# Kernel optimization log

Measured on AMD Instinct MI355X. Metric: run time of the kernel, lower is better.

## Reference

```python
import jax, jax.numpy as jnp
import numpy as np

N_ATOMS = 16384
N_SPECIES = 4
D_IN = 2880      # len(species)^2 * max_radial^2 * (max_angular+1) = 16*36*5
H = 256
N_STRUCTURES = 64


def setup_inputs() -> dict:
    key = jax.random.key(0)
    ks = jax.random.split(key, 9)
    features = jax.random.normal(ks[0], (N_ATOMS, D_IN), dtype=jnp.float32)
    # per-species MLP (MLPMap): 2 hidden layers with SiLU, then LinearMap -> 1
    w1 = jax.random.normal(ks[1], (N_SPECIES, D_IN, H), dtype=jnp.float32) * 0.02
    b1 = jax.random.normal(ks[2], (N_SPECIES, H), dtype=jnp.float32) * 0.02
    w2 = jax.random.normal(ks[3], (N_SPECIES, H, H), dtype=jnp.float32) * 0.05
    b2 = jax.random.normal(ks[4], (N_SPECIES, H), dtype=jnp.float32) * 0.02
    w_last = jax.random.normal(ks[5], (N_SPECIES, H), dtype=jnp.float32) * 0.05
    b_last = jax.random.normal(ks[6], (N_SPECIES,), dtype=jnp.float32) * 0.02
    comp_weights = jax.random.normal(ks[7], (N_SPECIES,), dtype=jnp.float32)
    # atoms are species-contiguous (TensorMap blocks); structures sorted
    structure_idx = jnp.sort(
        jax.random.randint(ks[8], (N_ATOMS,), 0, N_STRUCTURES, dtype=jnp.int32)
    )
    return {
        "features": features,
        "w1": w1, "b1": b1, "w2": w2, "b2": b2,
        "w_last": w_last, "b_last": b_last,
        "comp_weights": comp_weights,
        "structure_idx": structure_idx,
    }


def reference(features, w1, b1, w2, b2, w_last, b_last, comp_weights, structure_idx):
    S = N_SPECIES
    n_per = N_ATOMS // S
    # species-partitioned blocks: [S, n_per, D] — grouped GEMM form of the
    # per-species ModuleDict loop in MLPMap / LinearMap
    xs = features.reshape(S, n_per, D_IN)
    h = jax.nn.silu(jnp.einsum("snd,sdh->snh", xs, w1) + b1[:, None, :])
    h = jax.nn.silu(jnp.einsum("snh,shk->snk", h, w2) + b2[:, None, :])
    # LinearMap: per-species Linear(H, 1)
    e = jnp.einsum("snh,sh->sn", h, w_last) + b_last[:, None]  # [S, n_per]
    # apply_composition_contribution: add per-species composition weight
    species_per_atom = jnp.repeat(jnp.arange(S), n_per)
    atomic_energy = e.reshape(N_ATOMS) + comp_weights[species_per_atom]
    # keys_to_samples + sum_over_samples(['center','species_center'])
    total = jax.ops.segment_sum(atomic_energy, structure_idx,
                                num_segments=N_STRUCTURES)
    return total[:, None]  # [n_structures, 1] energy block
```

## Files before the change

### kernel.cpp

```cpp
#include <hip/hip_runtime.h>
#include <hip/hip_bf16.h>

#define D_IN    2880
#define HDIM    256
#define NSPEC   4
#define NATOMS  16384
#define NSTRUCT 64
#define NT1     45
#define NT2     4
#define BM      64

typedef __attribute__((ext_vector_type(4))) float f32x4;
typedef __attribute__((ext_vector_type(8))) short s16x8;
typedef __attribute__((ext_vector_type(4))) unsigned short u16x4;

__device__ __forceinline__ short f2bf(float f) {
    return (short)__builtin_bit_cast(unsigned short, __float2bfloat16(f));
}

template<int RDIM>
__global__ void pack_w(const float* __restrict__ w, unsigned short* __restrict__ wp) {
    __shared__ unsigned short T[64][264];
    const int kt = blockIdx.x, s = blockIdx.y;
    const int t = threadIdx.x;
    const float* src = w + ((size_t)s * RDIM + kt * 64) * HDIM;
#pragma unroll
    for (int i = 0; i < 16; ++i) {
        const int row = i * 4 + (t >> 6);
        const int c4 = (t & 63) * 4;
        f32x4 v = *(const f32x4*)(src + (size_t)row * HDIM + c4);
        u16x4 u;
        u[0] = (unsigned short)f2bf(v[0]); u[1] = (unsigned short)f2bf(v[1]);
        u[2] = (unsigned short)f2bf(v[2]); u[3] = (unsigned short)f2bf(v[3]);
        *(u16x4*)&T[row][c4] = u;
    }
    __syncthreads();
    unsigned short* dst = wp + ((size_t)s * (RDIM / 64) + kt) * 16384;
    const int l = t & 63;
#pragma unroll
    for (int it = 0; it < 8; ++it) {
        const int c = (t >> 6) + it * 4;
        const int hq = c >> 1, kk = c & 1;
        s16x8 vv;
#pragma unroll
        for (int e = 0; e < 8; ++e)
            vv[e] = (short)T[kk * 32 + (l >> 4) * 8 + e][hq * 16 + (l & 15)];
        *(s16x8*)(dst + (size_t)c * 512 + l * 8) = vv;
    }
}

__device__ __forceinline__ int aswz(int row, int colbyte) {
    return row * 128 + (colbyte ^ ((row & 7) << 4));
}
__device__ __forceinline__ int hswz(int row, int colbyte) {
    return row * 512 + (colbyte ^ ((row & 7) << 4));
}

__global__ __launch_bounds__(512, 2)
void fused_mlp(const float* __restrict__ feat,
               const unsigned short* __restrict__ w1p,
               const float* __restrict__ b1,
               const unsigned short* __restrict__ w2p,
               const float* __restrict__ b2,
               const float* __restrict__ w_last,
               const float* __restrict__ b_last,
               const float* __restrict__ comp_w,
               const int* __restrict__ sidx,
               float* __restrict__ out)
{
    __shared__ __align__(16) char Ab[2][8192];
    __shared__ __align__(16) char Hb[BM * 512];
    __shared__ float ered[4][BM];

    const int tid  = threadIdx.x;
    const int lane = tid & 63;
    const int wv   = tid >> 6;
    const int wr   = wv >> 2, wc = wv & 3;
    const int lrow = lane & 15, lq = lane >> 4;
    const int g    = blockIdx.x;
    const int s    = (g & 7) >> 1;
    const int mloc = ((g >> 3) << 1) | (g & 1);
    const int row0 = s * (NATOMS / NSPEC) + mloc * BM;

    const float* Ag = feat + (size_t)row0 * D_IN;
    const unsigned short* B1 = w1p + (size_t)s * NT1 * 16384;
    const unsigned short* B2 = w2p + (size_t)s * NT2 * 16384;

    const int ar  = tid >> 3;
    const int acb = (tid & 7) * 16;
    const int awo = aswz(ar, acb);

    f32x4 acc[2][4];
#pragma unroll
    for (int i = 0; i < 2; ++i)
#pragma unroll
        for (int j = 0; j < 4; ++j) acc[i][j] = (f32x4){0.f, 0.f, 0.f, 0.f};

    {
        const float* ap = Ag + (size_t)ar * D_IN + (tid & 7) * 8;
        f32x4 v0 = *(const f32x4*)ap;
        f32x4 v1 = *(const f32x4*)(ap + 4);
        s16x8 pw;
        pw[0]=f2bf(v0[0]); pw[1]=f2bf(v0[1]); pw[2]=f2bf(v0[2]); pw[3]=f2bf(v0[3]);
        pw[4]=f2bf(v1[0]); pw[5]=f2bf(v1[1]); pw[6]=f2bf(v1[2]); pw[7]=f2bf(v1[3]);
        *(s16x8*)(&Ab[0][0] + awo) = pw;
    }
    s16x8 Bf[2][4][2];
#pragma unroll
    for (int j = 0; j < 4; ++j)
#pragma unroll
        for (int kk = 0; kk < 2; ++kk)
            Bf[0][j][kk] = *(const s16x8*)(B1 + ((wc * 4 + j) * 2 + kk) * 512 + lane * 8);
    __syncthreads();

#pragma unroll 2
    for (int kt = 0; kt < NT1; ++kt) {
        const int cb = kt & 1, nb = cb ^ 1;
        const bool hn = (kt + 1) < NT1;
        f32x4 a0, a1;
        if (hn) {
            const float* ap = Ag + (size_t)ar * D_IN + (kt + 1) * 64 + (tid & 7) * 8;
            a0 = *(const f32x4*)ap;
            a1 = *(const f32x4*)(ap + 4);
#pragma unroll
            for (int j = 0; j < 4; ++j)
#pragma unroll
                for (int kk = 0; kk < 2; ++kk)
                    Bf[nb][j][kk] = *(const s16x8*)(B1 + ((size_t)(kt + 1) * 32 + (wc * 4 + j) * 2 + kk) * 512 + lane * 8);
        }
        s16x8 af[2][2];
#pragma unroll
        for (int i = 0; i < 2; ++i)
#pragma unroll
            for (int kk = 0; kk < 2; ++kk)
                af[i][kk] = *(const s16x8*)(&Ab[cb][0] + aswz(wr * 32 + i * 16 + lrow, kk * 64 + lq * 16));
#pragma unroll
        for (int kk = 0; kk < 2; ++kk)
#pragma unroll
            for (int i = 0; i < 2; ++i)
#pragma unroll
                for (int j = 0; j < 4; ++j)
                    acc[i][j] = __builtin_amdgcn_mfma_f32_16x16x32_bf16(af[i][kk], Bf[cb][j][kk], acc[i][j], 0, 0, 0);
        if (hn) {
            s16x8 pw;
            pw[0]=f2bf(a0[0]); pw[1]=f2bf(a0[1]); pw[2]=f2bf(a0[2]); pw[3]=f2bf(a0[3]);
            pw[4]=f2bf(a1[0]); pw[5]=f2bf(a1[1]); pw[6]=f2bf(a1[2]); pw[7]=f2bf(a1[3]);
            *(s16x8*)(&Ab[nb][0] + awo) = pw;
        }
        __syncthreads();
    }

    {
        const float* b1s = b1 + s * HDIM;
#pragma unroll
        for (int j = 0; j < 4; ++j) {
            const int col = wc * 64 + j * 16 + lrow;
            const float bias = b1s[col];
#pragma unroll
            for (int i = 0; i < 2; ++i)
#pragma unroll
                for (int r = 0; r < 4; ++r) {
                    float x = acc[i][j][r] + bias;
                    float sg = 1.0f / (1.0f + __expf(-x));
                    const int row = wr * 32 + i * 16 + lq * 4 + r;
                    *(unsigned short*)(&Hb[0] + hswz(row, col * 2)) = (unsigned short)f2bf(x * sg);
                }
        }
    }
#pragma unroll
    for (int i = 0; i < 2; ++i)
#pragma unroll
        for (int j = 0; j < 4; ++j) acc[i][j] = (f32x4){0.f, 0.f, 0.f, 0.f};

    s16x8 B2f[2][4][2];
#pragma unroll
    for (int j = 0; j < 4; ++j)
#pragma unroll
        for (int kk = 0; kk < 2; ++kk)
            B2f[0][j][kk] = *(const s16x8*)(B2 + ((wc * 4 + j) * 2 + kk) * 512 + lane * 8);
    __syncthreads();

#pragma unroll
    for (int kt = 0; kt < NT2; ++kt) {
        const int cb = kt & 1, nb = cb ^ 1;
        if (kt + 1 < NT2) {
#pragma unroll
            for (int j = 0; j < 4; ++j)
#pragma unroll
                for (int kk = 0; kk < 2; ++kk)
                    B2f[nb][j][kk] = *(const s16x8*)(B2 + ((size_t)(kt + 1) * 32 + (wc * 4 + j) * 2 + kk) * 512 + lane * 8);
        }
        s16x8 af[2][2];
#pragma unroll
        for (int i = 0; i < 2; ++i)
#pragma unroll
            for (int kk = 0; kk < 2; ++kk)
                af[i][kk] = *(const s16x8*)(&Hb[0] + hswz(wr * 32 + i * 16 + lrow, kt * 128 + kk * 64 + lq * 16));
#pragma unroll
        for (int kk = 0; kk < 2; ++kk)
#pragma unroll
            for (int i = 0; i < 2; ++i)
#pragma unroll
                for (int j = 0; j < 4; ++j)
                    acc[i][j] = __builtin_amdgcn_mfma_f32_16x16x32_bf16(af[i][kk], B2f[cb][j][kk], acc[i][j], 0, 0, 0);
    }

    {
        const float* b2s = b2 + s * HDIM;
        const float* wls = w_last + s * HDIM;
        float p[8];
#pragma unroll
        for (int t = 0; t < 8; ++t) p[t] = 0.f;
#pragma unroll
        for (int j = 0; j < 4; ++j) {
            const int col = wc * 64 + j * 16 + lrow;
            const float bias = b2s[col];
            const float wl = wls[col];
#pragma unroll
            for (int i = 0; i < 2; ++i)
#pragma unroll
                for (int r = 0; r < 4; ++r) {
                    float x = acc[i][j][r] + bias;
                    float sg = 1.0f / (1.0f + __expf(-x));
                    p[i * 4 + r] += x * sg * wl;
                }
        }
#pragma unroll
        for (int d = 1; d < 16; d <<= 1)
#pragma unroll
            for (int t = 0; t < 8; ++t)
                p[t] += __shfl_xor(p[t], d, 64);
        if (lrow == 0) {
#pragma unroll
            for (int i = 0; i < 2; ++i)
#pragma unroll
                for (int r = 0; r < 4; ++r)
                    ered[wc][wr * 32 + i * 16 + lq * 4 + r] = p[i * 4 + r];
        }
        __syncthreads();
        if (tid < BM) {
            float e = ered[0][tid] + ered[1][tid] + ered[2][tid] + ered[3][tid]
                    + b_last[s] + comp_w[s];
            atomicAdd(&out[sidx[row0 + tid]], e);
        }
    }
}

extern "C" void kernel_launch(void* const* d_in, const int* in_sizes, int n_in,
                              void* d_out, int out_size, void* d_ws, size_t ws_size,
                              hipStream_t stream) {
    (void)in_sizes; (void)n_in; (void)out_size; (void)ws_size;
    const float* feat   = (const float*)d_in[0];
    const float* w1     = (const float*)d_in[1];
    const float* b1     = (const float*)d_in[2];
    const float* w2     = (const float*)d_in[3];
    const float* b2     = (const float*)d_in[4];
    const float* w_last = (const float*)d_in[5];
    const float* b_last = (const float*)d_in[6];
    const float* comp_w = (const float*)d_in[7];
    const int*   sidx   = (const int*)d_in[8];
    float* out = (float*)d_out;

    unsigned short* w1p = (unsigned short*)d_ws;
    unsigned short* w2p = w1p + (size_t)NSPEC * NT1 * 16384;

    hipMemsetAsync(d_out, 0, NSTRUCT * sizeof(float), stream);
    pack_w<D_IN><<<dim3(NT1, NSPEC), 256, 0, stream>>>(w1, w1p);
    pack_w<HDIM><<<dim3(NT2, NSPEC), 256, 0, stream>>>(w2, w2p);
    fused_mlp<<<256, 512, 0, stream>>>(feat, w1p, b1, w2p, b2,
                                       w_last, b_last, comp_w, sidx, out);
}
```

Baseline: 403.9 us.

## Shrink row tile to 32, load A directly into registers without LDS staging

Halves the atom tile per block to 32 rows with 4 waves, doubling the grid to 512 blocks. The A operand is now read from global memory straight into MFMA fragments in registers, replacing the LDS double buffer and the per-iteration barrier. Software prefetch of the A and B fragments is removed in both GEMM loops. The aim is more blocks and no barrier stalls, at the cost of each wave re-reading the same A rows (four times per block), reading the w1 weights twice as often across the grid, and losing load/compute overlap.

```diff
diff --git a/kernel.cpp b/kernel.cpp
--- a/kernel.cpp
+++ b/kernel.cpp
@@ -8,7 +8,6 @@
 #define NSTRUCT 64
 #define NT1     45
 #define NT2     4
-#define BM      64
 
 typedef __attribute__((ext_vector_type(4))) float f32x4;
 typedef __attribute__((ext_vector_type(8))) short s16x8;
@@ -49,14 +48,11 @@
     }
 }
 
-__device__ __forceinline__ int aswz(int row, int colbyte) {
-    return row * 128 + (colbyte ^ ((row & 7) << 4));
-}
 __device__ __forceinline__ int hswz(int row, int colbyte) {
     return row * 512 + (colbyte ^ ((row & 7) << 4));
 }
 
-__global__ __launch_bounds__(512, 2)
+__global__ __launch_bounds__(256, 2)
 void fused_mlp(const float* __restrict__ feat,
                const unsigned short* __restrict__ w1p,
                const float* __restrict__ b1,
@@ -68,93 +64,62 @@
                const int* __restrict__ sidx,
                float* __restrict__ out)
 {
-    __shared__ __align__(16) char Ab[2][8192];
-    __shared__ __align__(16) char Hb[BM * 512];
-    __shared__ float ered[4][BM];
+    __shared__ __align__(16) char Hb[32 * 512];
+    __shared__ float ered[4][32];
 
     const int tid  = threadIdx.x;
     const int lane = tid & 63;
     const int wv   = tid >> 6;
-    const int wr   = wv >> 2, wc = wv & 3;
     const int lrow = lane & 15, lq = lane >> 4;
     const int g    = blockIdx.x;
     const int s    = (g & 7) >> 1;
-    const int mloc = ((g >> 3) << 1) | (g & 1);
-    const int row0 = s * (NATOMS / NSPEC) + mloc * BM;
+    const int idx  = ((g >> 3) << 1) | (g & 1);
+    const int row0 = s * (NATOMS / NSPEC) + idx * 32;
 
     const float* Ag = feat + (size_t)row0 * D_IN;
     const unsigned short* B1 = w1p + (size_t)s * NT1 * 16384;
     const unsigned short* B2 = w2p + (size_t)s * NT2 * 16384;
 
-    const int ar  = tid >> 3;
-    const int acb = (tid & 7) * 16;
-    const int awo = aswz(ar, acb);
-
     f32x4 acc[2][4];
 #pragma unroll
     for (int i = 0; i < 2; ++i)
 #pragma unroll
         for (int j = 0; j < 4; ++j) acc[i][j] = (f32x4){0.f, 0.f, 0.f, 0.f};
 
-    {
-        const float* ap = Ag + (size_t)ar * D_IN + (tid & 7) * 8;
-        f32x4 v0 = *(const f32x4*)ap;
-        f32x4 v1 = *(const f32x4*)(ap + 4);
-        s16x8 pw;
-        pw[0]=f2bf(v0[0]); pw[1]=f2bf(v0[1]); pw[2]=f2bf(v0[2]); pw[3]=f2bf(v0[3]);
-        pw[4]=f2bf(v1[0]); pw[5]=f2bf(v1[1]); pw[6]=f2bf(v1[2]); pw[7]=f2bf(v1[3]);
-        *(s16x8*)(&Ab[0][0] + awo) = pw;
-    }
-    s16x8 Bf[2][4][2];
-#pragma unroll
-    for (int j = 0; j < 4; ++j)
+    for (int kt = 0; kt < NT1; ++kt) {
+        s16x8 bf[4][2];
+#pragma unroll
+        for (int j = 0; j < 4; ++j)
+#pragma unroll
+            for (int kk = 0; kk < 2; ++kk)
+                bf[j][kk] = *(const s16x8*)(B1 + ((size_t)kt * 32 + (wv * 4 + j) * 2 + kk) * 512 + lane * 8);
+        s16x8 af[2][2];
+#pragma unroll
+        for (int i = 0; i < 2; ++i)
+#pragma unroll
+            for (int kk = 0; kk < 2; ++kk) {
+                const float* ap = Ag + (size_t)(i * 16 + lrow) * D_IN + kt * 64 + kk * 32 + lq * 8;
+                f32x4 v0 = *(const f32x4*)ap;
+                f32x4 v1 = *(const f32x4*)(ap + 4);
+                s16x8 w;
+                w[0]=f2bf(v0[0]); w[1]=f2bf(v0[1]); w[2]=f2bf(v0[2]); w[3]=f2bf(v0[3]);
+                w[4]=f2bf(v1[0]); w[5]=f2bf(v1[1]); w[6]=f2bf(v1[2]); w[7]=f2bf(v1[3]);
+                af[i][kk] = w;
+            }
 #pragma unroll
         for (int kk = 0; kk < 2; ++kk)
-            Bf[0][j][kk] = *(const s16x8*)(B1 + ((wc * 4 + j) * 2 + kk) * 512 + lane * 8);
-    __syncthreads();
-
-#pragma unroll 2
-    for (int kt = 0; kt < NT1; ++kt) {
-        const int cb = kt & 1, nb = cb ^ 1;
-        const bool hn = (kt + 1) < NT1;
-        f32x4 a0, a1;
-        if (hn) {
-            const float* ap = Ag + (size_t)ar * D_IN + (kt + 1) * 64 + (tid & 7) * 8;
-            a0 = *(const f32x4*)ap;
-            a1 = *(const f32x4*)(ap + 4);
-#pragma unroll
-            for (int j = 0; j < 4; ++j)
-#pragma unroll
-                for (int kk = 0; kk < 2; ++kk)
-                    Bf[nb][j][kk] = *(const s16x8*)(B1 + ((size_t)(kt + 1) * 32 + (wc * 4 + j) * 2 + kk) * 512 + lane * 8);
-        }
-        s16x8 af[2][2];
-#pragma unroll
-        for (int i = 0; i < 2; ++i)
-#pragma unroll
-            for (int kk = 0; kk < 2; ++kk)
-                af[i][kk] = *(const s16x8*)(&Ab[cb][0] + aswz(wr * 32 + i * 16 + lrow, kk * 64 + lq * 16));
-#pragma unroll
-        for (int kk = 0; kk < 2; ++kk)
 #pragma unroll
             for (int i = 0; i < 2; ++i)
 #pragma unroll
                 for (int j = 0; j < 4; ++j)
-                    acc[i][j] = __builtin_amdgcn_mfma_f32_16x16x32_bf16(af[i][kk], Bf[cb][j][kk], acc[i][j], 0, 0, 0);
-        if (hn) {
-            s16x8 pw;
-            pw[0]=f2bf(a0[0]); pw[1]=f2bf(a0[1]); pw[2]=f2bf(a0[2]); pw[3]=f2bf(a0[3]);
-            pw[4]=f2bf(a1[0]); pw[5]=f2bf(a1[1]); pw[6]=f2bf(a1[2]); pw[7]=f2bf(a1[3]);
-            *(s16x8*)(&Ab[nb][0] + awo) = pw;
-        }
-        __syncthreads();
+                    acc[i][j] = __builtin_amdgcn_mfma_f32_16x16x32_bf16(af[i][kk], bf[j][kk], acc[i][j], 0, 0, 0);
     }
 
     {
         const float* b1s = b1 + s * HDIM;
 #pragma unroll
         for (int j = 0; j < 4; ++j) {
-            const int col = wc * 64 + j * 16 + lrow;
+            const int col = wv * 64 + j * 16 + lrow;
             const float bias = b1s[col];
 #pragma unroll
             for (int i = 0; i < 2; ++i)
@@ -162,7 +127,7 @@
                 for (int r = 0; r < 4; ++r) {
                     float x = acc[i][j][r] + bias;
                     float sg = 1.0f / (1.0f + __expf(-x));
-                    const int row = wr * 32 + i * 16 + lq * 4 + r;
+                    const int row = i * 16 + lq * 4 + r;
                     *(unsigned short*)(&Hb[0] + hswz(row, col * 2)) = (unsigned short)f2bf(x * sg);
                 }
         }
@@ -171,38 +136,29 @@
     for (int i = 0; i < 2; ++i)
 #pragma unroll
         for (int j = 0; j < 4; ++j) acc[i][j] = (f32x4){0.f, 0.f, 0.f, 0.f};
-
-    s16x8 B2f[2][4][2];
-#pragma unroll
-    for (int j = 0; j < 4; ++j)
+    __syncthreads();
+
+#pragma unroll
+    for (int kt = 0; kt < NT2; ++kt) {
+        s16x8 bf[4][2];
+#pragma unroll
+        for (int j = 0; j < 4; ++j)
+#pragma unroll
+            for (int kk = 0; kk < 2; ++kk)
+                bf[j][kk] = *(const s16x8*)(B2 + ((size_t)kt * 32 + (wv * 4 + j) * 2 + kk) * 512 + lane * 8);
+        s16x8 af[2][2];
+#pragma unroll
+        for (int i = 0; i < 2; ++i)
+#pragma unroll
+            for (int kk = 0; kk < 2; ++kk)
+                af[i][kk] = *(const s16x8*)(&Hb[0] + hswz(i * 16 + lrow, (kt * 64 + kk * 32 + lq * 8) * 2));
 #pragma unroll
         for (int kk = 0; kk < 2; ++kk)
-            B2f[0][j][kk] = *(const s16x8*)(B2 + ((wc * 4 + j) * 2 + kk) * 512 + lane * 8);
-    __syncthreads();
-
-#pragma unroll
-    for (int kt = 0; kt < NT2; ++kt) {
-        const int cb = kt & 1, nb = cb ^ 1;
-        if (kt + 1 < NT2) {
-#pragma unroll
-            for (int j = 0; j < 4; ++j)
-#pragma unroll
-                for (int kk = 0; kk < 2; ++kk)
-                    B2f[nb][j][kk] = *(const s16x8*)(B2 + ((size_t)(kt + 1) * 32 + (wc * 4 + j) * 2 + kk) * 512 + lane * 8);
-        }
-        s16x8 af[2][2];
-#pragma unroll
-        for (int i = 0; i < 2; ++i)
-#pragma unroll
-            for (int kk = 0; kk < 2; ++kk)
-                af[i][kk] = *(const s16x8*)(&Hb[0] + hswz(wr * 32 + i * 16 + lrow, kt * 128 + kk * 64 + lq * 16));
-#pragma unroll
-        for (int kk = 0; kk < 2; ++kk)
 #pragma unroll
             for (int i = 0; i < 2; ++i)
 #pragma unroll
                 for (int j = 0; j < 4; ++j)
-                    acc[i][j] = __builtin_amdgcn_mfma_f32_16x16x32_bf16(af[i][kk], B2f[cb][j][kk], acc[i][j], 0, 0, 0);
+                    acc[i][j] = __builtin_amdgcn_mfma_f32_16x16x32_bf16(af[i][kk], bf[j][kk], acc[i][j], 0, 0, 0);
     }
 
     {
@@ -213,7 +169,7 @@
         for (int t = 0; t < 8; ++t) p[t] = 0.f;
 #pragma unroll
         for (int j = 0; j < 4; ++j) {
-            const int col = wc * 64 + j * 16 + lrow;
+            const int col = wv * 64 + j * 16 + lrow;
             const float bias = b2s[col];
             const float wl = wls[col];
 #pragma unroll
@@ -235,10 +191,10 @@
             for (int i = 0; i < 2; ++i)
 #pragma unroll
                 for (int r = 0; r < 4; ++r)
-                    ered[wc][wr * 32 + i * 16 + lq * 4 + r] = p[i * 4 + r];
+                    ered[wv][i * 16 + lq * 4 + r] = p[i * 4 + r];
         }
         __syncthreads();
-        if (tid < BM) {
+        if (tid < 32) {
             float e = ered[0][tid] + ered[1][tid] + ered[2][tid] + ered[3][tid]
                     + b_last[s] + comp_w[s];
             atomicAdd(&out[sidx[row0 + tid]], e);
@@ -267,6 +223,6 @@
     hipMemsetAsync(d_out, 0, NSTRUCT * sizeof(float), stream);
     pack_w<D_IN><<<dim3(NT1, NSPEC), 256, 0, stream>>>(w1, w1p);
     pack_w<HDIM><<<dim3(NT2, NSPEC), 256, 0, stream>>>(w2, w2p);
-    fused_mlp<<<256, 512, 0, stream>>>(feat, w1p, b1, w2p, b2,
+    fused_mlp<<<512, 256, 0, stream>>>(feat, w1p, b1, w2p, b2,
                                        w_last, b_last, comp_w, sidx, out);
 }
```

Result: slower. 466.1 us (+15.4%).
